# Optimization experiments

Hardware: AMD Instinct MI355X
Metric: run time of the kernel (lower is better)

Reference implementation:

```python
import jax, jax.numpy as jnp
import numpy as np

BATCH, SEQ, D_MODEL = 4, 4096, 1024
HEADS, DIM_HEAD = 8, 128
BUCKET, N_HASHES = 64, 4
N_BUCKETS = SEQ // BUCKET
LN_EPS = 1e-3
SELF_ATTN_VAL = -5e4   # TOKEN_SELF_ATTN_VALUE in reformer_pytorch
MASK_VAL = -1e9        # stand-in for max_neg_value on padded keys
UNIT_EPS = 1e-6        # make_unit_length epsilon


def setup_inputs() -> dict:
    key = jax.random.key(0)
    ks = jax.random.split(key, 8)
    s = 0.02
    return {
        "i": jax.random.normal(ks[0], (BATCH, SEQ, D_MODEL), jnp.float32),
        "mask": jnp.ones((BATCH, SEQ), dtype=bool),
        "rotations": jax.random.normal(ks[1], (DIM_HEAD, N_HASHES, N_BUCKETS // 2), jnp.float32),
        "Wqk": jax.random.normal(ks[2], (D_MODEL, D_MODEL), jnp.float32) * s,
        "Wv": jax.random.normal(ks[3], (D_MODEL, D_MODEL), jnp.float32) * s,
        "Wo": jax.random.normal(ks[4], (D_MODEL, D_MODEL), jnp.float32) * s,
        "bo": jnp.zeros((D_MODEL,), jnp.float32),
        "ln_g": jnp.ones((D_MODEL,), jnp.float32),
        "ln_b": jnp.zeros((D_MODEL,), jnp.float32),
    }


def _look_one_back(x):
    # concat each chunk with the previous chunk along the within-chunk axis
    return jnp.concatenate([x, jnp.roll(x, 1, axis=1)], axis=2)


def _lsh_attention(qk, v, mask, rotations):
    # qk, v: (B, T, d) with B = batch*heads; mask: (B, T) bool
    B, T, d = qk.shape
    # --- hash into buckets (no grad through hashing) ---
    rot = jnp.einsum('btd,dhr->bhtr', jax.lax.stop_gradient(qk), rotations)
    rot = jnp.concatenate([rot, -rot], axis=-1)              # (B, nh, T, n_buckets)
    buckets = jnp.argmax(rot, axis=-1)                       # (B, nh, T)
    offsets = (jnp.arange(N_HASHES) * N_BUCKETS)[None, :, None]
    buckets = (buckets + offsets).reshape(B, N_HASHES * T)
    # --- stable bucket sort of tokens ---
    ticker = jnp.arange(N_HASHES * T)
    buckets_and_t = buckets * T + (ticker % T)               # unique keys
    sticker = jnp.argsort(buckets_and_t, axis=-1)            # (B, nh*T)
    undo_sort = jnp.argsort(sticker, axis=-1)
    st = sticker % T                                         # original positions
    sqk = jnp.take_along_axis(qk, st[..., None], axis=1)
    sv = jnp.take_along_axis(v, st[..., None], axis=1)
    # --- chunked local attention ---
    n_chunks = N_HASHES * N_BUCKETS
    bq_t = st.reshape(B, n_chunks, BUCKET)
    bq = sqk.reshape(B, n_chunks, BUCKET, d)
    nrm = jnp.linalg.norm(bq, axis=-1, keepdims=True)
    bk = bq / jnp.maximum(nrm, UNIT_EPS)                     # shared-QK: keys are unit-length queries
    bv = sv.reshape(B, n_chunks, BUCKET, d)
    bk = _look_one_back(bk)                                  # (B, C, 2*BUCKET, d)
    bv = _look_one_back(bv)
    bkv_t = _look_one_back(bq_t)                             # (B, C, 2*BUCKET)
    dots = jnp.einsum('bcid,bcjd->bcij', bq, bk) * (d ** -0.5)
    # input (padding) mask
    mq = jnp.take_along_axis(mask, st, axis=1).reshape(B, n_chunks, BUCKET)
    mkv = _look_one_back(mq)
    dots = jnp.where(mq[..., :, None] & mkv[..., None, :], dots, MASK_VAL)
    # avoid attending to self except as a fallback
    dots = jnp.where(bq_t[..., :, None] == bkv_t[..., None, :], SELF_ATTN_VAL, dots)
    dots_lse = jax.nn.logsumexp(dots, axis=-1, keepdims=True)  # (B, C, BUCKET, 1)
    probs = jnp.exp(dots - dots_lse)
    bo = jnp.einsum('bcij,bcjd->bcid', probs, bv)
    so = bo.reshape(B, N_HASHES * T, d)
    slogits = dots_lse.reshape(B, N_HASHES * T)
    # --- unsort and combine hash rounds via softmax over per-round logsumexps ---
    o = jnp.take_along_axis(so, undo_sort[..., None], axis=1).reshape(B, N_HASHES, T, d)
    logits = jnp.take_along_axis(slogits, undo_sort, axis=1).reshape(B, N_HASHES, T, 1)
    w = jnp.exp(logits - jax.nn.logsumexp(logits, axis=1, keepdims=True))
    return jnp.sum(o * w, axis=1)                            # (B, T, d)


def _forward(i, mask, rotations, Wqk, Wv, Wo, bo, ln_g, ln_b):
    b, t, dm = i.shape
    qk = i @ Wqk
    v = i @ Wv

    def split_heads(x):
        return x.reshape(b, t, HEADS, DIM_HEAD).transpose(0, 2, 1, 3).reshape(b * HEADS, t, DIM_HEAD)

    qk, v = split_heads(qk), split_heads(v)
    m = jnp.repeat(mask, HEADS, axis=0)                      # (b*h, t)
    out = _lsh_attention(qk, v, m, rotations)
    out = out.reshape(b, HEADS, t, DIM_HEAD).transpose(0, 2, 1, 3).reshape(b, t, dm)
    out = out @ Wo + bo                                      # to_out
    # eval-mode dropout is identity; then LayerNorm(eps=1e-3)
    mu = out.mean(-1, keepdims=True)
    var = out.var(-1, keepdims=True)
    return (out - mu) / jnp.sqrt(var + LN_EPS) * ln_g + ln_b


def reference(i, mask, rotations, Wqk, Wv, Wo, bo, ln_g, ln_b):
    return _forward(i, mask, rotations, Wqk, Wv, Wo, bo, ln_g, ln_b)
```

## Files before the change

### kernel.cpp

```cpp
#include <hip/hip_runtime.h>
#include <hip/hip_bf16.h>

#define B_   4
#define T_   4096
#define DM   1024
#define H_   8
#define DH   128
#define BHN  32
#define NH   4
#define NB   64
#define NT   16384
#define NC   256
#define SCALE_ 0.08838834764831845f
#define SELF_VAL -50000.0f
#define FLAG_CAP 262144
#define GAP_THR 2.5e-3f

typedef unsigned short u16;
typedef __attribute__((ext_vector_type(8))) short short8;
typedef __attribute__((ext_vector_type(8))) unsigned short us8;
typedef __attribute__((ext_vector_type(4))) float f32x4;

__device__ __forceinline__ float bf2f(u16 x) {
  union { unsigned u; float f; } c; c.u = ((unsigned)x) << 16; return c.f;
}
__device__ __forceinline__ u16 f2bf(float f) {
  union { float f; unsigned u; } c; c.f = f;
  unsigned r = (c.u + 0x7FFFu + ((c.u >> 16) & 1u)) >> 16;
  return (u16)r;
}
__device__ __forceinline__ void gload16(const void* g, void* l) {
  __builtin_amdgcn_global_load_lds(
      (const __attribute__((address_space(1))) void*)g,
      (__attribute__((address_space(3))) void*)l, 16, 0, 0);
}

__global__ __launch_bounds__(256) void k_isplit(
    const float* __restrict__ I, u16* __restrict__ ih, u16* __restrict__ il) {
  size_t idx = ((size_t)blockIdx.x * 256 + threadIdx.x) * 8;
  us8 vh, vl;
  #pragma unroll
  for (int e = 0; e < 8; ++e) {
    float x = I[idx + e];
    u16 h = f2bf(x);
    vh[e] = h;
    vl[e] = f2bf(x - bf2f(h));
  }
  *(us8*)(ih + idx) = vh;
  *(us8*)(il + idx) = vl;
}

__global__ __launch_bounds__(256) void k_wr(
    const float* __restrict__ Wqk, const float* __restrict__ R, double* __restrict__ WR) {
  __shared__ float lR[128][128];
  int tid = threadIdx.x;
  int k0 = blockIdx.x * 64, h = blockIdx.y;
  #pragma unroll
  for (int q = 0; q < 64; ++q)
    ((float*)lR)[q * 256 + tid] = R[q * 256 + tid];
  __syncthreads();
  int k = k0 + (tid >> 2);
  int hr0 = (tid & 3) * 32;
  double acc[32];
  #pragma unroll
  for (int j = 0; j < 32; ++j) acc[j] = 0.0;
  for (int d = 0; d < 128; ++d) {
    double w = (double)Wqk[(size_t)k * DM + h * DH + d];
    #pragma unroll
    for (int j = 0; j < 32; ++j)
      acc[j] = fma(w, (double)lR[d][hr0 + j], acc[j]);
  }
  double* o = WR + ((size_t)h * 1024 + k) * 128 + hr0;
  #pragma unroll
  for (int j = 0; j < 32; ++j) o[j] = acc[j];
}

__global__ __launch_bounds__(256) void k_wsplit(
    const float* __restrict__ Wqk, const float* __restrict__ Wv,
    const float* __restrict__ Wo, const double* __restrict__ WR,
    u16* __restrict__ Wqkt, u16* __restrict__ Wvt, u16* __restrict__ Wot,
    u16* __restrict__ WR2t) {
  int tid = blockIdx.x * 256 + threadIdx.x;
  int k = tid >> 7, n8 = (tid & 127) << 3;
  #pragma unroll
  for (int j = 0; j < 8; ++j) {
    int n = n8 + j;
    Wqkt[(size_t)n * 1024 + k] = f2bf(Wqk[(size_t)k * 1024 + n]);
    Wvt [(size_t)n * 1024 + k] = f2bf(Wv [(size_t)k * 1024 + n]);
    Wot [(size_t)n * 1024 + k] = f2bf(Wo [(size_t)k * 1024 + n]);
    double w = WR[((size_t)(n >> 7) * 1024 + k) * 128 + (n & 127)];
    u16 wh = f2bf((float)w);
    u16 wl = f2bf((float)(w - (double)bf2f(wh)));
    WR2t[(size_t)n * 2048 + k] = wh;
    WR2t[(size_t)n * 2048 + 1024 + k] = wl;
  }
}

__global__ void k_zero(unsigned* flagc) { if (threadIdx.x == 0) *flagc = 0; }

template <int EPI>
__global__ __launch_bounds__(256) void k_gemm(
    const u16* __restrict__ A, const u16* __restrict__ A2,
    const u16* __restrict__ Bt, int K,
    u16* __restrict__ outb, float* __restrict__ outf, const float* __restrict__ bias,
    int* __restrict__ buckets, unsigned* __restrict__ flagc, int* __restrict__ flags) {
  __shared__ char smem[34816];
  u16 (*smA)[64] = (u16 (*)[64])smem;
  u16 (*smB)[64] = (u16 (*)[64])(smem + 16384);
  int tid = threadIdx.x;
  int m0 = blockIdx.x * 128, n0 = blockIdx.y * 128;
  int w = tid >> 6, lane = tid & 63;
  int wr = w >> 1, wc = w & 1;
  int arow = lane & 15, kg = lane >> 4;
  const int ldb = (EPI == 2) ? 2048 : 1024;
  int lrow = lane >> 3;
  int gch = (lane & 7) ^ lrow;

  f32x4 acc[4][4];
  #pragma unroll
  for (int m = 0; m < 4; ++m)
    #pragma unroll
    for (int n = 0; n < 4; ++n) acc[m][n] = (f32x4){0.f, 0.f, 0.f, 0.f};

  int axor = (arow & 7) << 3;

  auto run_seg = [&](const u16* Ab, const u16* Bb) {
    for (int kk = 0; kk < 1024; kk += 64) {
      __syncthreads();
      #pragma unroll
      for (int q = 0; q < 4; ++q) {
        int row = q * 32 + w * 8 + lrow;
        gload16(Ab + (size_t)(m0 + row) * 1024 + kk + gch * 8,
                smem + (q * 4096 + w * 1024));
        gload16(Bb + (size_t)(n0 + row) * ldb + kk + gch * 8,
                smem + 16384 + (q * 4096 + w * 1024));
      }
      __syncthreads();
      #pragma unroll
      for (int ks = 0; ks < 2; ++ks) {
        short8 af[4], bf[4];
        #pragma unroll
        for (int m = 0; m < 4; ++m)
          af[m] = *(const short8*)(&smA[wr * 64 + m * 16 + arow][((ks * 4 + kg) << 3) ^ axor]);
        #pragma unroll
        for (int n = 0; n < 4; ++n)
          bf[n] = *(const short8*)(&smB[wc * 64 + n * 16 + arow][((ks * 4 + kg) << 3) ^ axor]);
        #pragma unroll
        for (int m = 0; m < 4; ++m)
          #pragma unroll
          for (int n = 0; n < 4; ++n)
            acc[m][n] = __builtin_amdgcn_mfma_f32_16x16x32_bf16(af[m], bf[n], acc[m][n], 0, 0, 0);
      }
    }
  };

  if constexpr (EPI == 2) {
    run_seg(A, Bt);
    run_seg(A, Bt + 1024);
    run_seg(A2, Bt);
  } else {
    run_seg(A, Bt);
  }

  if constexpr (EPI == 0) {
    #pragma unroll
    for (int m = 0; m < 4; ++m)
      #pragma unroll
      for (int n = 0; n < 4; ++n)
        #pragma unroll
        for (int r = 0; r < 4; ++r) {
          int orow = wr * 64 + m * 16 + kg * 4 + r;
          int ocol = wc * 64 + n * 16 + arow;
          outb[(size_t)(m0 + orow) * 1024 + n0 + ocol] = f2bf(acc[m][n][r]);
        }
  } else if constexpr (EPI == 1) {
    #pragma unroll
    for (int m = 0; m < 4; ++m)
      #pragma unroll
      for (int n = 0; n < 4; ++n)
        #pragma unroll
        for (int r = 0; r < 4; ++r) {
          int orow = wr * 64 + m * 16 + kg * 4 + r;
          int ocol = wc * 64 + n * 16 + arow;
          outf[(size_t)(m0 + orow) * 1024 + n0 + ocol] = acc[m][n][r] + bias[n0 + ocol];
        }
  } else {
    float (*sC)[132] = (float (*)[132])smem;
    #pragma unroll
    for (int pass = 0; pass < 2; ++pass) {
      __syncthreads();
      if (wr == pass) {
        #pragma unroll
        for (int m = 0; m < 4; ++m)
          #pragma unroll
          for (int n = 0; n < 4; ++n)
            #pragma unroll
            for (int r = 0; r < 4; ++r)
              sC[m * 16 + kg * 4 + r][wc * 64 + n * 16 + arow] = acc[m][n][r];
      }
      __syncthreads();
      int tok = tid >> 2, hash = tid & 3;
      const float* rw = &sC[tok][hash * 32];
      float m1 = -3.4e38f, m2 = -3.4e38f; int bi = 0;
      #pragma unroll
      for (int j = 0; j < 32; ++j) {
        float vv = rw[j];
        if (vv > m1) { m2 = m1; m1 = vv; bi = j; }
        else if (vv > m2) m2 = vv;
      }
      #pragma unroll
      for (int j = 0; j < 32; ++j) {
        float vv = -rw[j];
        if (vv > m1) { m2 = m1; m1 = vv; bi = 32 + j; }
        else if (vv > m2) m2 = vv;
      }
      int bt = m0 + pass * 64 + tok;
      int b = bt >> 12, t = bt & 4095;
      buckets[((size_t)(b * 8 + blockIdx.y) * 4 + hash) * T_ + t] = bi;
      if (m1 - m2 < GAP_THR) {
        unsigned pos = atomicAdd(flagc, 1u);
        if (pos < FLAG_CAP) flags[pos] = (bt << 5) | ((int)blockIdx.y << 2) | hash;
      }
    }
  }
}

__global__ __launch_bounds__(64) void k_fb(
    const float* __restrict__ I, const double* __restrict__ WR,
    const unsigned* __restrict__ flagc, const int* __restrict__ flags,
    int* __restrict__ buckets) {
  unsigned n = *flagc; if (n > FLAG_CAP) n = FLAG_CAP;
  int lane = threadIdx.x;
  for (unsigned it = blockIdx.x; it < n; it += gridDim.x) {
    int f = flags[it];
    int bt = f >> 5, h = (f >> 2) & 7, hash = f & 3;
    int j = lane & 31, half = lane >> 5;
    const float* ip = I + (size_t)bt * 1024 + half * 512;
    const double* wp = WR + ((size_t)h * 1024 + half * 512) * 128 + hash * 32 + j;
    double acc = 0.0;
    for (int k = 0; k < 512; ++k)
      acc = fma((double)ip[k], wp[(size_t)k * 128], acc);
    acc += __shfl_down(acc, 32, 64);
    double bv = acc; int bi = j;
    double vneg = -acc;
    if (vneg > bv) { bv = vneg; bi = 32 + j; }
    #pragma unroll
    for (int m = 1; m < 32; m <<= 1) {
      double ov = __shfl_xor(bv, m, 64);
      int oi = __shfl_xor(bi, m, 64);
      if (ov > bv || (ov == bv && oi < bi)) { bv = ov; bi = oi; }
    }
    if (lane == 0) {
      int b = bt >> 12, t = bt & 4095;
      buckets[((size_t)(b * 8 + h) * 4 + hash) * T_ + t] = bi;
    }
  }
}

__global__ __launch_bounds__(64) void k_sort(
    const int* __restrict__ buckets, int* __restrict__ st, int* __restrict__ inv) {
  __shared__ int hist[64][65];
  __shared__ int base[64];
  int bh = blockIdx.x, r = blockIdx.y;
  int m = threadIdx.x;
  #pragma unroll
  for (int b = 0; b < 64; ++b) hist[b][m] = 0;
  __syncthreads();
  const int* bk = buckets + ((size_t)bh * NH + r) * T_;
  for (int q = 0; q < 64; ++q) hist[bk[m * 64 + q]][m]++;
  __syncthreads();
  {
    int run = 0;
    for (int c = 0; c < 64; ++c) { int x = hist[m][c]; hist[m][c] = run; run += x; }
    base[m] = run;
  }
  __syncthreads();
  if (m == 0) {
    int s = 0;
    for (int b = 0; b < 64; ++b) { int x = base[b]; base[b] = s; s += x; }
  }
  __syncthreads();
  int* stb = st + (size_t)bh * NT + (size_t)r * T_;
  int* ivb = inv + (size_t)bh * NT + (size_t)r * T_;
  for (int q = 0; q < 64; ++q) {
    int t = m * 64 + q;
    int b = bk[t];
    int pos = base[b] + hist[b][m]++;
    stb[pos] = t;
    ivb[t] = r * T_ + pos;
  }
}

__global__ __launch_bounds__(256) void k_attn(
    const u16* __restrict__ qk, const u16* __restrict__ V, const int* __restrict__ st,
    u16* __restrict__ o_s, float* __restrict__ slog) {
  __shared__ u16 kbuf[128][136];
  __shared__ u16 pbuf[64][136];
  __shared__ int tks[128];
  float* psum   = (float*)&pbuf[0][0];
  float* recipn = (float*)&pbuf[4][0];
  int tid = threadIdx.x;
  int bh = blockIdx.x, chunk = blockIdx.y;
  int bb_ = bh >> 3, hh_ = bh & 7;
  const int* stb = st + (size_t)bh * NT;
  if (tid < 128) {
    int j = tid;
    int p = (j < 64) ? (chunk * 64 + j)
                     : (((chunk + NC - 1) % NC) * 64 + (j - 64));
    tks[j] = stb[p];
  }
  __syncthreads();
  {
    int j = tid & 127, half = tid >> 7;
    const ushort4* rp = (const ushort4*)(qk + ((size_t)(bb_ * T_ + tks[j])) * DM + hh_ * DH + half * 64);
    ushort4* dp = (ushort4*)(&kbuf[j][half * 64]);
    float ss = 0.f;
    #pragma unroll
    for (int c = 0; c < 16; ++c) {
      ushort4 x = rp[c];
      float f0 = bf2f(x.x), f1 = bf2f(x.y), f2 = bf2f(x.z), f3 = bf2f(x.w);
      ss += f0 * f0 + f1 * f1 + f2 * f2 + f3 * f3;
      dp[c] = x;
    }
    psum[j * 2 + half] = ss;
  }
  __syncthreads();
  if (tid < 128) {
    float n = sqrtf(psum[tid * 2] + psum[tid * 2 + 1]);
    recipn[tid] = 1.f / fmaxf(n, 1e-6f);
  }
  __syncthreads();

  int w = tid >> 6, lane = tid & 63;
  int arow = lane & 15, kgrp = lane >> 4;

  f32x4 acc[8];
  #pragma unroll
  for (int n = 0; n < 8; ++n) acc[n] = (f32x4){0.f, 0.f, 0.f, 0.f};
  #pragma unroll
  for (int kk = 0; kk < 4; ++kk) {
    short8 a = *(const short8*)(&kbuf[w * 16 + arow][kk * 32 + kgrp * 8]);
    #pragma unroll
    for (int n = 0; n < 8; ++n) {
      short8 bb = *(const short8*)(&kbuf[n * 16 + arow][kk * 32 + kgrp * 8]);
      acc[n] = __builtin_amdgcn_mfma_f32_16x16x32_bf16(a, bb, acc[n], 0, 0, 0);
    }
  }

  int ti[4];
  #pragma unroll
  for (int r = 0; r < 4; ++r) ti[r] = tks[w * 16 + kgrp * 4 + r];
  float vals[8][4];
  float rmax[4] = {-3.0e38f, -3.0e38f, -3.0e38f, -3.0e38f};
  #pragma unroll
  for (int n = 0; n < 8; ++n) {
    int j = n * 16 + arow;
    float rc = recipn[j] * SCALE_;
    int tj = tks[j];
    #pragma unroll
    for (int r = 0; r < 4; ++r) {
      float d = acc[n][r] * rc;
      if (ti[r] == tj) d = SELF_VAL;
      vals[n][r] = d;
      rmax[r] = fmaxf(rmax[r], d);
    }
  }
  __syncthreads();
  #pragma unroll
  for (int m = 1; m <= 8; m <<= 1) {
    #pragma unroll
    for (int r = 0; r < 4; ++r) rmax[r] = fmaxf(rmax[r], __shfl_xor(rmax[r], m, 64));
  }
  float rsum[4] = {0.f, 0.f, 0.f, 0.f};
  #pragma unroll
  for (int n = 0; n < 8; ++n) {
    #pragma unroll
    for (int r = 0; r < 4; ++r) {
      float e = __expf(vals[n][r] - rmax[r]);
      vals[n][r] = e;
      rsum[r] += e;
    }
  }
  #pragma unroll
  for (int m = 1; m <= 8; m <<= 1) {
    #pragma unroll
    for (int r = 0; r < 4; ++r) rsum[r] += __shfl_xor(rsum[r], m, 64);
  }
  float rinv[4], lse[4];
  #pragma unroll
  for (int r = 0; r < 4; ++r) {
    rinv[r] = 1.f / rsum[r];
    lse[r] = rmax[r] + __logf(rsum[r]);
  }
  if (arow == 0) {
    #pragma unroll
    for (int r = 0; r < 4; ++r)
      slog[(size_t)bh * NT + chunk * 64 + w * 16 + kgrp * 4 + r] = lse[r];
  }
  #pragma unroll
  for (int n = 0; n < 8; ++n) {
    #pragma unroll
    for (int r = 0; r < 4; ++r)
      pbuf[w * 16 + kgrp * 4 + r][n * 16 + arow] = f2bf(vals[n][r] * rinv[r]);
  }
  __syncthreads();
  {
    int j = tid & 127, half = tid >> 7;
    const ushort4* rp = (const ushort4*)(V + ((size_t)(bb_ * T_ + tks[j])) * DM + hh_ * DH + half * 64);
    #pragma unroll
    for (int c = 0; c < 16; ++c) {
      ushort4 x = rp[c];
      int d = half * 64 + c * 4;
      kbuf[d + 0][j] = x.x;
      kbuf[d + 1][j] = x.y;
      kbuf[d + 2][j] = x.z;
      kbuf[d + 3][j] = x.w;
    }
  }
  __syncthreads();

  f32x4 acc2[8];
  #pragma unroll
  for (int n = 0; n < 8; ++n) acc2[n] = (f32x4){0.f, 0.f, 0.f, 0.f};
  #pragma unroll
  for (int kk = 0; kk < 4; ++kk) {
    short8 a = *(const short8*)(&pbuf[w * 16 + arow][kk * 32 + kgrp * 8]);
    #pragma unroll
    for (int n = 0; n < 8; ++n) {
      short8 bb = *(const short8*)(&kbuf[n * 16 + arow][kk * 32 + kgrp * 8]);
      acc2[n] = __builtin_amdgcn_mfma_f32_16x16x32_bf16(a, bb, acc2[n], 0, 0, 0);
    }
  }
  u16* ob = o_s + ((size_t)bh * NT + (size_t)chunk * 64) * DH;
  #pragma unroll
  for (int n = 0; n < 8; ++n) {
    #pragma unroll
    for (int r = 0; r < 4; ++r)
      ob[(size_t)(w * 16 + kgrp * 4 + r) * DH + n * 16 + arow] = f2bf(acc2[n][r]);
  }
}

__global__ __launch_bounds__(256) void k_comb(
    const u16* __restrict__ o_s, const float* __restrict__ slog,
    const int* __restrict__ inv, u16* __restrict__ attn) {
  int tid = threadIdx.x;
  int bh = blockIdx.y;
  int t = blockIdx.x * 2 + (tid >> 7);
  int dd = tid & 127;
  const int* ivb = inv + (size_t)bh * NT;
  int p[4]; float l[4];
  #pragma unroll
  for (int r = 0; r < 4; ++r) {
    p[r] = ivb[r * T_ + t];
    l[r] = slog[(size_t)bh * NT + p[r]];
  }
  float m = fmaxf(fmaxf(l[0], l[1]), fmaxf(l[2], l[3]));
  float wv[4]; float wsum = 0.f;
  #pragma unroll
  for (int r = 0; r < 4; ++r) { wv[r] = __expf(l[r] - m); wsum += wv[r]; }
  float rs = 1.f / wsum;
  float o = 0.f;
  #pragma unroll
  for (int r = 0; r < 4; ++r)
    o += wv[r] * bf2f(o_s[((size_t)bh * NT + p[r]) * DH + dd]);
  o *= rs;
  int b = bh >> 3, h = bh & 7;
  attn[((size_t)(b * T_ + t)) * DM + h * DH + dd] = f2bf(o);
}

__global__ __launch_bounds__(256) void k_ln(
    const float* __restrict__ X, const float* __restrict__ G,
    const float* __restrict__ Bt, float* __restrict__ out) {
  __shared__ float w1[4], w2[4];
  int row = blockIdx.x, tid = threadIdx.x;
  const float4 v = ((const float4*)(X + (size_t)row * DM))[tid];
  float s = v.x + v.y + v.z + v.w;
  float s2 = v.x * v.x + v.y * v.y + v.z * v.z + v.w * v.w;
  #pragma unroll
  for (int m = 1; m < 64; m <<= 1) {
    s += __shfl_xor(s, m, 64);
    s2 += __shfl_xor(s2, m, 64);
  }
  int wid = tid >> 6;
  if ((tid & 63) == 0) { w1[wid] = s; w2[wid] = s2; }
  __syncthreads();
  float S = w1[0] + w1[1] + w1[2] + w1[3];
  float S2 = w2[0] + w2[1] + w2[2] + w2[3];
  float mu = S * (1.f / DM);
  float var = S2 * (1.f / DM) - mu * mu;
  float inv = 1.0f / sqrtf(var + 1e-3f);
  float4 g = ((const float4*)G)[tid];
  float4 b = ((const float4*)Bt)[tid];
  float4 o;
  o.x = (v.x - mu) * inv * g.x + b.x;
  o.y = (v.y - mu) * inv * g.y + b.y;
  o.z = (v.z - mu) * inv * g.z + b.z;
  o.w = (v.w - mu) * inv * g.w + b.w;
  ((float4*)(out + (size_t)row * DM))[tid] = o;
}

extern "C" void kernel_launch(void* const* d_in, const int* in_sizes, int n_in,
                              void* d_out, int out_size, void* d_ws, size_t ws_size,
                              hipStream_t stream) {
  const float* I   = (const float*)d_in[0];
  const float* R   = (const float*)d_in[2];
  const float* Wqk = (const float*)d_in[3];
  const float* Wv  = (const float*)d_in[4];
  const float* Wo  = (const float*)d_in[5];
  const float* bo  = (const float*)d_in[6];
  const float* lng = (const float*)d_in[7];
  const float* lnb = (const float*)d_in[8];

  char* ws = (char*)d_ws;
  const size_t MB = 1ull << 20;
  u16*      qk      = (u16*)(ws + 0);
  u16*      v       = (u16*)(ws + 32 * MB);
  u16*      o_s     = (u16*)(ws + 64 * MB);
  u16*      i_hi    = (u16*)(ws + 64 * MB);
  u16*      i_lo    = (u16*)(ws + 96 * MB);
  double*   WR      = (double*)(ws + 128 * MB);
  int*      flags   = (int*)(ws + 136 * MB);
  unsigned* flagc   = (unsigned*)(ws + 137 * MB);
  int*      buckets = (int*)(ws + 138 * MB);
  u16*      Wqkt    = (u16*)(ws + 140 * MB);
  u16*      Wvt     = (u16*)(ws + 142 * MB);
  u16*      WR2t    = (u16*)(ws + 144 * MB);
  float*    outp    = (float*)(ws + 64 * MB);
  int*      st      = (int*)(ws + 192 * MB);
  int*      inv     = (int*)(ws + 194 * MB);
  float*    slog    = (float*)(ws + 196 * MB);
  u16*      Wot     = (u16*)(ws + 198 * MB);
  u16*      attnb   = qk;
  float*    out     = (float*)d_out;

  k_isplit<<<8192, 256, 0, stream>>>(I, i_hi, i_lo);
  k_wr<<<dim3(16, 8), 256, 0, stream>>>(Wqk, R, WR);
  k_wsplit<<<512, 256, 0, stream>>>(Wqk, Wv, Wo, WR, Wqkt, Wvt, Wot, WR2t);
  k_zero<<<1, 64, 0, stream>>>(flagc);
  k_gemm<0><<<dim3(128, 8), 256, 0, stream>>>(i_hi, nullptr, Wqkt, 1024, qk, nullptr, nullptr, nullptr, nullptr, nullptr);
  k_gemm<0><<<dim3(128, 8), 256, 0, stream>>>(i_hi, nullptr, Wvt, 1024, v, nullptr, nullptr, nullptr, nullptr, nullptr);
  k_gemm<2><<<dim3(128, 8), 256, 0, stream>>>(i_hi, i_lo, WR2t, 3072, nullptr, nullptr, nullptr, buckets, flagc, flags);
  k_fb<<<1024, 64, 0, stream>>>(I, WR, flagc, flags, buckets);
  k_sort<<<dim3(BHN, NH), 64, 0, stream>>>(buckets, st, inv);
  k_attn<<<dim3(BHN, NC), 256, 0, stream>>>(qk, v, st, o_s, slog);
  k_comb<<<dim3(T_ / 2, BHN), 256, 0, stream>>>(o_s, slog, inv, attnb);
  k_gemm<1><<<dim3(128, 8), 256, 0, stream>>>(attnb, nullptr, Wot, 1024, nullptr, outp, bo, nullptr, nullptr, nullptr);
  k_ln<<<B_ * T_, 256, 0, stream>>>(outp, lng, lnb, out);
}
```

Before: 562.9 us.

## Fuse QK/V projections and scatter attention outputs to unsorted order

Concatenates Wqk and Wv into one transposed weight so a single GEMM launch produces both qk and v. The attention kernel now writes per-round outputs and logsumexps directly to original token positions, so the sort no longer builds an inverse permutation. The combine kernel then reads contiguously and handles 16 tokens per block. MFMA sections get raised wave priority. The attention stores become scattered instead of contiguous.

```diff
diff --git a/kernel.cpp b/kernel.cpp
--- a/kernel.cpp
+++ b/kernel.cpp
@@ -78,16 +78,15 @@
 __global__ __launch_bounds__(256) void k_wsplit(
     const float* __restrict__ Wqk, const float* __restrict__ Wv,
     const float* __restrict__ Wo, const double* __restrict__ WR,
-    u16* __restrict__ Wqkt, u16* __restrict__ Wvt, u16* __restrict__ Wot,
-    u16* __restrict__ WR2t) {
+    u16* __restrict__ Wqkvt, u16* __restrict__ Wot, u16* __restrict__ WR2t) {
   int tid = blockIdx.x * 256 + threadIdx.x;
   int k = tid >> 7, n8 = (tid & 127) << 3;
   #pragma unroll
   for (int j = 0; j < 8; ++j) {
     int n = n8 + j;
-    Wqkt[(size_t)n * 1024 + k] = f2bf(Wqk[(size_t)k * 1024 + n]);
-    Wvt [(size_t)n * 1024 + k] = f2bf(Wv [(size_t)k * 1024 + n]);
-    Wot [(size_t)n * 1024 + k] = f2bf(Wo [(size_t)k * 1024 + n]);
+    Wqkvt[(size_t)n * 1024 + k]          = f2bf(Wqk[(size_t)k * 1024 + n]);
+    Wqkvt[(size_t)(1024 + n) * 1024 + k] = f2bf(Wv [(size_t)k * 1024 + n]);
+    Wot  [(size_t)n * 1024 + k]          = f2bf(Wo [(size_t)k * 1024 + n]);
     double w = WR[((size_t)(n >> 7) * 1024 + k) * 128 + (n & 127)];
     u16 wh = f2bf((float)w);
     u16 wl = f2bf((float)(w - (double)bf2f(wh)));
@@ -101,8 +100,9 @@
 template <int EPI>
 __global__ __launch_bounds__(256) void k_gemm(
     const u16* __restrict__ A, const u16* __restrict__ A2,
-    const u16* __restrict__ Bt, int K,
-    u16* __restrict__ outb, float* __restrict__ outf, const float* __restrict__ bias,
+    const u16* __restrict__ Bt,
+    u16* __restrict__ outb, u16* __restrict__ outb2,
+    float* __restrict__ outf, const float* __restrict__ bias,
     int* __restrict__ buckets, unsigned* __restrict__ flagc, int* __restrict__ flags) {
   __shared__ char smem[34816];
   u16 (*smA)[64] = (u16 (*)[64])smem;
@@ -163,6 +163,8 @@
   }
 
   if constexpr (EPI == 0) {
+    u16* dst = (n0 < 1024) ? outb : outb2;
+    int nc0 = (n0 < 1024) ? n0 : (n0 - 1024);
     #pragma unroll
     for (int m = 0; m < 4; ++m)
       #pragma unroll
@@ -171,7 +173,7 @@
         for (int r = 0; r < 4; ++r) {
           int orow = wr * 64 + m * 16 + kg * 4 + r;
           int ocol = wc * 64 + n * 16 + arow;
-          outb[(size_t)(m0 + orow) * 1024 + n0 + ocol] = f2bf(acc[m][n][r]);
+          dst[(size_t)(m0 + orow) * 1024 + nc0 + ocol] = f2bf(acc[m][n][r]);
         }
   } else if constexpr (EPI == 1) {
     #pragma unroll
@@ -258,7 +260,7 @@
 }
 
 __global__ __launch_bounds__(64) void k_sort(
-    const int* __restrict__ buckets, int* __restrict__ st, int* __restrict__ inv) {
+    const int* __restrict__ buckets, int* __restrict__ st) {
   __shared__ int hist[64][65];
   __shared__ int base[64];
   int bh = blockIdx.x, r = blockIdx.y;
@@ -281,19 +283,17 @@
   }
   __syncthreads();
   int* stb = st + (size_t)bh * NT + (size_t)r * T_;
-  int* ivb = inv + (size_t)bh * NT + (size_t)r * T_;
   for (int q = 0; q < 64; ++q) {
     int t = m * 64 + q;
     int b = bk[t];
     int pos = base[b] + hist[b][m]++;
     stb[pos] = t;
-    ivb[t] = r * T_ + pos;
   }
 }
 
 __global__ __launch_bounds__(256) void k_attn(
     const u16* __restrict__ qk, const u16* __restrict__ V, const int* __restrict__ st,
-    u16* __restrict__ o_s, float* __restrict__ slog) {
+    u16* __restrict__ o_u, float* __restrict__ slog_u) {
   __shared__ u16 kbuf[128][136];
   __shared__ u16 pbuf[64][136];
   __shared__ int tks[128];
@@ -301,6 +301,7 @@
   float* recipn = (float*)&pbuf[4][0];
   int tid = threadIdx.x;
   int bh = blockIdx.x, chunk = blockIdx.y;
+  int round = chunk >> 6;
   int bb_ = bh >> 3, hh_ = bh & 7;
   const int* stb = st + (size_t)bh * NT;
   if (tid < 128) {
@@ -337,6 +338,7 @@
   f32x4 acc[8];
   #pragma unroll
   for (int n = 0; n < 8; ++n) acc[n] = (f32x4){0.f, 0.f, 0.f, 0.f};
+  __builtin_amdgcn_s_setprio(1);
   #pragma unroll
   for (int kk = 0; kk < 4; ++kk) {
     short8 a = *(const short8*)(&kbuf[w * 16 + arow][kk * 32 + kgrp * 8]);
@@ -346,6 +348,7 @@
       acc[n] = __builtin_amdgcn_mfma_f32_16x16x32_bf16(a, bb, acc[n], 0, 0, 0);
     }
   }
+  __builtin_amdgcn_s_setprio(0);
 
   int ti[4];
   #pragma unroll
@@ -395,7 +398,7 @@
   if (arow == 0) {
     #pragma unroll
     for (int r = 0; r < 4; ++r)
-      slog[(size_t)bh * NT + chunk * 64 + w * 16 + kgrp * 4 + r] = lse[r];
+      slog_u[((size_t)(bh * NH + round)) * T_ + ti[r]] = lse[r];
   }
   #pragma unroll
   for (int n = 0; n < 8; ++n) {
@@ -422,6 +425,7 @@
   f32x4 acc2[8];
   #pragma unroll
   for (int n = 0; n < 8; ++n) acc2[n] = (f32x4){0.f, 0.f, 0.f, 0.f};
+  __builtin_amdgcn_s_setprio(1);
   #pragma unroll
   for (int kk = 0; kk < 4; ++kk) {
     short8 a = *(const short8*)(&pbuf[w * 16 + arow][kk * 32 + kgrp * 8]);
@@ -431,41 +435,43 @@
       acc2[n] = __builtin_amdgcn_mfma_f32_16x16x32_bf16(a, bb, acc2[n], 0, 0, 0);
     }
   }
-  u16* ob = o_s + ((size_t)bh * NT + (size_t)chunk * 64) * DH;
+  __builtin_amdgcn_s_setprio(0);
+  u16* ob = o_u + ((size_t)(bh * NH + round)) * T_ * DH;
   #pragma unroll
   for (int n = 0; n < 8; ++n) {
     #pragma unroll
     for (int r = 0; r < 4; ++r)
-      ob[(size_t)(w * 16 + kgrp * 4 + r) * DH + n * 16 + arow] = f2bf(acc2[n][r]);
+      ob[(size_t)ti[r] * DH + n * 16 + arow] = f2bf(acc2[n][r]);
   }
 }
 
 __global__ __launch_bounds__(256) void k_comb(
-    const u16* __restrict__ o_s, const float* __restrict__ slog,
-    const int* __restrict__ inv, u16* __restrict__ attn) {
+    const u16* __restrict__ o_u, const float* __restrict__ slog_u,
+    u16* __restrict__ attn) {
   int tid = threadIdx.x;
   int bh = blockIdx.y;
-  int t = blockIdx.x * 2 + (tid >> 7);
+  int t0 = blockIdx.x * 16;
   int dd = tid & 127;
-  const int* ivb = inv + (size_t)bh * NT;
-  int p[4]; float l[4];
-  #pragma unroll
-  for (int r = 0; r < 4; ++r) {
-    p[r] = ivb[r * T_ + t];
-    l[r] = slog[(size_t)bh * NT + p[r]];
-  }
-  float m = fmaxf(fmaxf(l[0], l[1]), fmaxf(l[2], l[3]));
-  float wv[4]; float wsum = 0.f;
-  #pragma unroll
-  for (int r = 0; r < 4; ++r) { wv[r] = __expf(l[r] - m); wsum += wv[r]; }
-  float rs = 1.f / wsum;
-  float o = 0.f;
-  #pragma unroll
-  for (int r = 0; r < 4; ++r)
-    o += wv[r] * bf2f(o_s[((size_t)bh * NT + p[r]) * DH + dd]);
-  o *= rs;
   int b = bh >> 3, h = bh & 7;
-  attn[((size_t)(b * T_ + t)) * DM + h * DH + dd] = f2bf(o);
+  #pragma unroll
+  for (int i = 0; i < 8; ++i) {
+    int t = t0 + (tid >> 7) + i * 2;
+    float l[4];
+    #pragma unroll
+    for (int r = 0; r < 4; ++r)
+      l[r] = slog_u[((size_t)(bh * NH + r)) * T_ + t];
+    float m = fmaxf(fmaxf(l[0], l[1]), fmaxf(l[2], l[3]));
+    float wv[4]; float wsum = 0.f;
+    #pragma unroll
+    for (int r = 0; r < 4; ++r) { wv[r] = __expf(l[r] - m); wsum += wv[r]; }
+    float rs = 1.f / wsum;
+    float o = 0.f;
+    #pragma unroll
+    for (int r = 0; r < 4; ++r)
+      o += wv[r] * bf2f(o_u[(((size_t)(bh * NH + r)) * T_ + t) * DH + dd]);
+    o *= rs;
+    attn[((size_t)(b * T_ + t)) * DM + h * DH + dd] = f2bf(o);
+  }
 }
 
 __global__ __launch_bounds__(256) void k_ln(
@@ -515,35 +521,32 @@
   const size_t MB = 1ull << 20;
   u16*      qk      = (u16*)(ws + 0);
   u16*      v       = (u16*)(ws + 32 * MB);
-  u16*      o_s     = (u16*)(ws + 64 * MB);
+  u16*      o_u     = (u16*)(ws + 64 * MB);
   u16*      i_hi    = (u16*)(ws + 64 * MB);
   u16*      i_lo    = (u16*)(ws + 96 * MB);
   double*   WR      = (double*)(ws + 128 * MB);
   int*      flags   = (int*)(ws + 136 * MB);
   unsigned* flagc   = (unsigned*)(ws + 137 * MB);
   int*      buckets = (int*)(ws + 138 * MB);
-  u16*      Wqkt    = (u16*)(ws + 140 * MB);
-  u16*      Wvt     = (u16*)(ws + 142 * MB);
+  u16*      Wqkvt   = (u16*)(ws + 140 * MB);
   u16*      WR2t    = (u16*)(ws + 144 * MB);
   float*    outp    = (float*)(ws + 64 * MB);
   int*      st      = (int*)(ws + 192 * MB);
-  int*      inv     = (int*)(ws + 194 * MB);
-  float*    slog    = (float*)(ws + 196 * MB);
+  float*    slog_u  = (float*)(ws + 196 * MB);
   u16*      Wot     = (u16*)(ws + 198 * MB);
   u16*      attnb   = qk;
   float*    out     = (float*)d_out;
 
   k_isplit<<<8192, 256, 0, stream>>>(I, i_hi, i_lo);
   k_wr<<<dim3(16, 8), 256, 0, stream>>>(Wqk, R, WR);
-  k_wsplit<<<512, 256, 0, stream>>>(Wqk, Wv, Wo, WR, Wqkt, Wvt, Wot, WR2t);
+  k_wsplit<<<512, 256, 0, stream>>>(Wqk, Wv, Wo, WR, Wqkvt, Wot, WR2t);
   k_zero<<<1, 64, 0, stream>>>(flagc);
-  k_gemm<0><<<dim3(128, 8), 256, 0, stream>>>(i_hi, nullptr, Wqkt, 1024, qk, nullptr, nullptr, nullptr, nullptr, nullptr);
-  k_gemm<0><<<dim3(128, 8), 256, 0, stream>>>(i_hi, nullptr, Wvt, 1024, v, nullptr, nullptr, nullptr, nullptr, nullptr);
-  k_gemm<2><<<dim3(128, 8), 256, 0, stream>>>(i_hi, i_lo, WR2t, 3072, nullptr, nullptr, nullptr, buckets, flagc, flags);
+  k_gemm<0><<<dim3(128, 16), 256, 0, stream>>>(i_hi, nullptr, Wqkvt, qk, v, nullptr, nullptr, nullptr, nullptr, nullptr);
+  k_gemm<2><<<dim3(128, 8), 256, 0, stream>>>(i_hi, i_lo, WR2t, nullptr, nullptr, nullptr, nullptr, buckets, flagc, flags);
   k_fb<<<1024, 64, 0, stream>>>(I, WR, flagc, flags, buckets);
-  k_sort<<<dim3(BHN, NH), 64, 0, stream>>>(buckets, st, inv);
-  k_attn<<<dim3(BHN, NC), 256, 0, stream>>>(qk, v, st, o_s, slog);
-  k_comb<<<dim3(T_ / 2, BHN), 256, 0, stream>>>(o_s, slog, inv, attnb);
-  k_gemm<1><<<dim3(128, 8), 256, 0, stream>>>(attnb, nullptr, Wot, 1024, nullptr, outp, bo, nullptr, nullptr, nullptr);
+  k_sort<<<dim3(BHN, NH), 64, 0, stream>>>(buckets, st);
+  k_attn<<<dim3(BHN, NC), 256, 0, stream>>>(qk, v, st, o_u, slog_u);
+  k_comb<<<dim3(T_ / 16, BHN), 256, 0, stream>>>(o_u, slog_u, attnb);
+  k_gemm<1><<<dim3(128, 8), 256, 0, stream>>>(attnb, nullptr, Wot, nullptr, nullptr, outp, bo, nullptr, nullptr, nullptr);
   k_ln<<<B_ * T_, 256, 0, stream>>>(outp, lng, lnb, out);
 }
```

New measurement: 533.3 us. 5.3% less time.
